# Performance work log

Measured on AMD Instinct MI355X. Metric: run time of the kernel, lower is better.

## Reference

```python
import jax, jax.numpy as jnp
import numpy as np

G = 64  # fixed grid size hardcoded in the torch module

def setup_inputs() -> dict:
    key = jax.random.key(0)
    ks = jax.random.split(key, 12)
    N, H = 500000, 256
    s = lambda fan_in: 1.0 / np.sqrt(fan_in)
    return {
        "positions": jax.random.normal(ks[0], (N, 3), jnp.float32) * 2.0,
        "grid_points": jax.random.normal(ks[1], (G, 3), jnp.float32) * 2.0,
        "W1": jax.random.normal(ks[2], (3, 64), jnp.float32) * s(3),
        "b1": jnp.zeros((64,), jnp.float32),
        "W2": jax.random.normal(ks[3], (64, 128), jnp.float32) * s(64),
        "b2": jnp.zeros((128,), jnp.float32),
        "W3": jax.random.normal(ks[4], (128, H), jnp.float32) * s(128),
        "b3": jnp.zeros((H,), jnp.float32),
        "Wn1": jax.random.normal(ks[5], (H, H), jnp.float32) * s(H),
        "bn1": jnp.zeros((H,), jnp.float32),
        "Wn2": jax.random.normal(ks[6], (H, H), jnp.float32) * s(H),
        "bn2": jnp.zeros((H,), jnp.float32),
        "Wh1": jax.random.normal(ks[7], (4, H, 128), jnp.float32) * s(H),
        "bh1": jnp.zeros((4, 128), jnp.float32),
        "Wh2": jax.random.normal(ks[8], (4, 128, 1), jnp.float32) * s(128),
        "bh2": jnp.zeros((4, 1), jnp.float32),
    }

def reference(positions, grid_points, W1, b1, W2, b2, W3, b3,
              Wn1, bn1, Wn2, bn2, Wh1, bh1, Wh2, bh2):
    # crystal_encoder: per-atom MLP 3 -> 64 -> 128 -> 256 over ALL N atoms
    h = jax.nn.relu(positions @ W1 + b1)
    h = jax.nn.relu(h @ W2 + b2)
    feat = h @ W3 + b3                                   # [N, H]

    # _map_crystal_to_grid: only the first min(N, 64) atoms are mapped.
    pos64 = positions[:G]                                # [64, 3]
    d2 = jnp.sum((pos64[:, None, :] - grid_points[None, :, :]) ** 2, axis=-1)
    idx = jnp.argmin(d2, axis=-1)                        # [64] nearest grid point per atom
    winner = jnp.full((G,), -1, jnp.int32).at[idx].max(jnp.arange(G, dtype=jnp.int32))
    grid_feats = jnp.where(winner[:, None] >= 0,
                           feat[jnp.clip(winner, 0)], 0.0)  # [64, H]

    # TetrahedralAGINetwork (per-node MLP, channels-first output convention)
    x = grid_feats[None]                                 # [1, 64, H]
    y = jax.nn.relu(x @ Wn1 + bn1) @ Wn2 + bn2           # [1, 64, H]
    agg = jnp.mean(jnp.swapaxes(y, 1, 2), axis=-1)       # mean over nodes -> [1, H]

    # 4 property heads, batched: [4, 1, 1] -> [4] (order: band_gap,
    # elastic_modulus, thermal_conductivity, dielectric_constant)
    h1 = jax.nn.relu(jnp.einsum('bc,kcd->kbd', agg, Wh1) + bh1[:, None, :])
    props = jnp.einsum('kbd,kdo->kbo', h1, Wh2) + bh2[:, None, :]
    return props.reshape(4)
```

## Files before the change

kernel.cpp:

```cpp
#include <hip/hip_runtime.h>


__device__ __forceinline__ void async_cp16(const float* g, float* l) {
    __builtin_amdgcn_global_load_lds(
        (const __attribute__((address_space(1))) void*)g,
        (__attribute__((address_space(3))) void*)l, 16, 0, 0);
}

__device__ __forceinline__ void stage_contig(const float* g, float* l, int nfloats, int tid) {
    const int lane = tid & 63, wv = tid >> 6;
    const int ninst = nfloats >> 8;
    for (int i = wv; i < ninst; i += 4)
        async_cp16(g + i*256 + lane*4, l + i*256);
}
__device__ __forceinline__ void stage_slice32(const float* g, float* l, int ld, int j0, int nrows, int tid) {
    const int lane = tid & 63, wv = tid >> 6;
    const int r = lane >> 3, c4 = (lane & 7) << 2;
    const int ninst = nrows >> 3;
    for (int i = wv; i < ninst; i += 4)
        async_cp16(g + (i*8 + r)*ld + j0 + c4, l + i*256);
}

__global__ __launch_bounds__(256) void k0_backbone(
    const float* __restrict__ positions, const float* __restrict__ grid,
    const float* __restrict__ W1, const float* __restrict__ b1,
    const float* __restrict__ W2, const float* __restrict__ b2,
    float* __restrict__ h2g_ws, int* __restrict__ win_ws)
{
    __shared__ __align__(16) float w2_s[64*128];
    __shared__ __align__(16) float h1_s[64][64];
    __shared__ float pos_s[192], grid_s[192], w1_s[192], b1_s[64];
    __shared__ int idx_s[64], win_s[64];

    const int tid = threadIdx.x;
    stage_contig(W2, w2_s, 64*128, tid);

    if (tid < 192) { pos_s[tid] = positions[tid]; grid_s[tid] = grid[tid]; w1_s[tid] = W1[tid]; }
    if (tid >= 192) b1_s[tid - 192] = b1[tid - 192];
    const float bb2 = b2[tid & 127];
    __syncthreads();

    if (tid < 64) {
        const float px = pos_s[tid*3], py = pos_s[tid*3+1], pz = pos_s[tid*3+2];
        float best = 3.4e38f; int bi = 0;
        for (int g = 0; g < 64; ++g) {
            const float dx = px - grid_s[g*3];
            const float dy = py - grid_s[g*3+1];
            const float dz = pz - grid_s[g*3+2];
            const float d2 = dx*dx + dy*dy + dz*dz;
            if (d2 < best) { best = d2; bi = g; }
        }
        idx_s[tid] = bi;
    }
    __syncthreads();
    if (tid < 64) {
        int m = -1;
        for (int i = 0; i < 64; ++i) if (idx_s[i] == tid) m = i;
        win_s[tid] = m;
        win_ws[tid] = m;
    }
    __syncthreads();

    #pragma unroll
    for (int u = 0; u < 16; ++u) {
        const int e = tid + u*256;
        const int t = e >> 6, k = e & 63;
        int r = win_s[t]; if (r < 0) r = 0;
        const float acc = b1_s[k] + pos_s[r*3]*w1_s[k] + pos_s[r*3+1]*w1_s[64+k]
                                  + pos_s[r*3+2]*w1_s[128+k];
        h1_s[t][k] = fmaxf(acc, 0.f);
    }
    __syncthreads();

    {
        const int d = tid & 127, t0 = tid >> 7;
        for (int bp = 0; bp < 8; ++bp) {
            float acc[4];
            #pragma unroll
            for (int m = 0; m < 4; ++m) acc[m] = bb2;
            for (int kc = 0; kc < 64; kc += 16) {
                float w[16];
                #pragma unroll
                for (int u = 0; u < 16; ++u) w[u] = w2_s[(kc+u)*128 + d];
                #pragma unroll
                for (int u = 0; u < 16; u += 4) {
                    #pragma unroll
                    for (int m = 0; m < 4; ++m) {
                        const float4 h4 = *(const float4*)&h1_s[bp*8 + t0 + 2*m][kc + u];
                        acc[m] += h4.x*w[u] + h4.y*w[u+1] + h4.z*w[u+2] + h4.w*w[u+3];
                    }
                }
            }
            #pragma unroll
            for (int m = 0; m < 4; ++m)
                h2g_ws[(bp*8 + t0 + 2*m)*128 + d] = fmaxf(acc[m], 0.f);
        }
    }
}

__global__ __launch_bounds__(256) void k1_gf(
    const float* __restrict__ W3, const float* __restrict__ b3,
    const float* __restrict__ h2g_ws, const int* __restrict__ win_ws,
    float* __restrict__ gf_ws)
{
    __shared__ __align__(16) float w3_s[128*32];
    __shared__ __align__(16) float h2_s[64*128];
    __shared__ int win_s[64];

    const int tid = threadIdx.x;
    const int j0  = blockIdx.x * 32;
    stage_slice32(W3, w3_s, 256, j0, 128, tid);
    stage_contig(h2g_ws, h2_s, 64*128, tid);

    const int jl = tid & 31, g = tid >> 5;
    const int j  = j0 + jl;
    const float bb = b3[j];
    if (tid < 64) win_s[tid] = win_ws[tid];
    __syncthreads();

    float acc[8];
    #pragma unroll
    for (int t = 0; t < 8; ++t) acc[t] = 0.f;
    for (int dc = 0; dc < 128; dc += 16) {
        float w[16];
        #pragma unroll
        for (int u = 0; u < 16; ++u) w[u] = w3_s[(dc+u)*32 + jl];
        #pragma unroll
        for (int u = 0; u < 16; u += 4) {
            #pragma unroll
            for (int t = 0; t < 8; ++t) {
                const float4 h4 = *(const float4*)&h2_s[(g*8 + t)*128 + dc + u];
                acc[t] += h4.x*w[u] + h4.y*w[u+1] + h4.z*w[u+2] + h4.w*w[u+3];
            }
        }
    }
    #pragma unroll
    for (int t = 0; t < 8; ++t)
        gf_ws[(g*8 + t)*256 + j] = (win_s[g*8 + t] >= 0) ? (acc[t] + bb) : 0.f;
}

__global__ __launch_bounds__(256) void k2_tpart(
    const float* __restrict__ Wn1, const float* __restrict__ bn1,
    const float* __restrict__ gf_ws, float* __restrict__ tpart_ws)
{
    __shared__ __align__(16) float wn1_s[256*32];
    __shared__ __align__(16) float gf_s[8*256];
    __shared__ float r_s[256];

    const int tid = threadIdx.x;
    const int bg  = blockIdx.x >> 3;
    const int j0  = (blockIdx.x & 7) * 32;
    stage_slice32(Wn1, wn1_s, 256, j0, 256, tid);
    stage_contig(gf_ws + bg*8*256, gf_s, 8*256, tid);

    const int jl = tid & 31, t = tid >> 5;
    const float bb = bn1[j0 + jl];
    __syncthreads();

    float acc = bb;
    for (int cc = 0; cc < 256; cc += 32) {
        float w[32];
        #pragma unroll
        for (int u = 0; u < 32; ++u) w[u] = wn1_s[(cc+u)*32 + jl];
        #pragma unroll
        for (int u = 0; u < 32; u += 4) {
            const float4 g4 = *(const float4*)&gf_s[t*256 + cc + u];
            acc += g4.x*w[u] + g4.y*w[u+1] + g4.z*w[u+2] + g4.w*w[u+3];
        }
    }
    r_s[tid] = fmaxf(acc, 0.f);
    __syncthreads();
    if (t == 0) {
        float ps = 0.f;
        #pragma unroll
        for (int tt = 0; tt < 8; ++tt) ps += r_s[tt*32 + jl];
        tpart_ws[bg*256 + j0 + jl] = ps;
    }
}

__global__ __launch_bounds__(256) void k3_agg(
    const float* __restrict__ Wn2, const float* __restrict__ bn2,
    const float* __restrict__ tpart_ws, float* __restrict__ agg_ws)
{
    __shared__ __align__(16) float wn2_s[256*32];
    __shared__ __align__(16) float tp_s[8*256];
    __shared__ __align__(16) float tbar_s[256];

    const int tid = threadIdx.x;
    const int c0  = blockIdx.x * 32;
    stage_slice32(Wn2, wn2_s, 256, c0, 256, tid);
    stage_contig(tpart_ws, tp_s, 8*256, tid);

    const float bb = (tid < 32) ? bn2[c0 + tid] : 0.f;
    __syncthreads();

    {
        float tb = 0.f;
        #pragma unroll
        for (int q = 0; q < 8; ++q) tb += tp_s[q*256 + tid];
        tbar_s[tid] = tb * (1.f/64.f);
    }
    __syncthreads();

    if (tid < 32) {
        float acc = bb;
        for (int jc = 0; jc < 256; jc += 32) {
            float w[32];
            #pragma unroll
            for (int u = 0; u < 32; ++u) w[u] = wn2_s[(jc+u)*32 + tid];
            #pragma unroll
            for (int u = 0; u < 32; u += 4) {
                const float4 t4 = *(const float4*)&tbar_s[jc + u];
                acc += t4.x*w[u] + t4.y*w[u+1] + t4.z*w[u+2] + t4.w*w[u+3];
            }
        }
        agg_ws[c0 + tid] = acc;
    }
}

__global__ __launch_bounds__(256) void k4_heads(
    const float* __restrict__ Wh1, const float* __restrict__ bh1,
    const float* __restrict__ agg_ws, float* __restrict__ h1h_ws)
{
    __shared__ __align__(16) float wh1_s[256*32];
    __shared__ __align__(16) float agg_s[256];

    const int tid = threadIdx.x;
    const int k   = blockIdx.x >> 2;
    const int d0  = (blockIdx.x & 3) * 32;
    stage_slice32(Wh1 + k*256*128, wh1_s, 128, d0, 256, tid);
    stage_contig(agg_ws, agg_s, 256, tid);

    const float bia = (tid < 32) ? bh1[k*128 + d0 + tid] : 0.f;
    __syncthreads();

    if (tid < 32) {
        float acc = bia;
        for (int cc = 0; cc < 256; cc += 16) {
            float wa[16];
            #pragma unroll
            for (int u = 0; u < 16; ++u) wa[u] = wh1_s[(cc+u)*32 + tid];
            #pragma unroll
            for (int u = 0; u < 16; u += 4) {
                const float4 a4 = *(const float4*)&agg_s[cc + u];
                acc += a4.x*wa[u] + a4.y*wa[u+1] + a4.z*wa[u+2] + a4.w*wa[u+3];
            }
        }
        h1h_ws[k*128 + d0 + tid] = fmaxf(acc, 0.f);
    }
}

__global__ __launch_bounds__(256) void k5_out(
    const float* __restrict__ Wh2, const float* __restrict__ bh2,
    const float* __restrict__ h1h_ws, float* __restrict__ out)
{
    __shared__ __align__(16) float h1h_s[512];
    __shared__ __align__(16) float wh2_s[512];
    const int tid = threadIdx.x;
    stage_contig(h1h_ws, h1h_s, 512, tid);
    stage_contig(Wh2,    wh2_s, 512, tid);
    const float bb = (tid < 4) ? bh2[tid] : 0.f;
    __syncthreads();

    if (tid < 4) {
        float acc = bb;
        for (int d = 0; d < 128; ++d) acc += h1h_s[tid*128 + d] * wh2_s[tid*128 + d];
        out[tid] = acc;
    }
}

extern "C" void kernel_launch(void* const* d_in, const int* in_sizes, int n_in,
                              void* d_out, int out_size, void* d_ws, size_t ws_size,
                              hipStream_t stream) {
    const float* positions = (const float*)d_in[0];
    const float* grid      = (const float*)d_in[1];
    const float* W1  = (const float*)d_in[2];
    const float* b1  = (const float*)d_in[3];
    const float* W2  = (const float*)d_in[4];
    const float* b2  = (const float*)d_in[5];
    const float* W3  = (const float*)d_in[6];
    const float* b3  = (const float*)d_in[7];
    const float* Wn1 = (const float*)d_in[8];
    const float* bn1 = (const float*)d_in[9];
    const float* Wn2 = (const float*)d_in[10];
    const float* bn2 = (const float*)d_in[11];
    const float* Wh1 = (const float*)d_in[12];
    const float* bh1 = (const float*)d_in[13];
    const float* Wh2 = (const float*)d_in[14];
    const float* bh2 = (const float*)d_in[15];
    float* out = (float*)d_out;

    char* ws = (char*)d_ws;
    float* h2g_ws   = (float*)(ws + 0);
    int*   win_ws   = (int*)  (ws + 32768);
    float* gf_ws    = (float*)(ws + 36864);
    float* tpart_ws = (float*)(ws + 102400);
    float* agg_ws   = (float*)(ws + 110592);
    float* h1h_ws   = (float*)(ws + 111616);

    hipLaunchKernelGGL(k0_backbone, dim3(1),  dim3(256), 0, stream,
                       positions, grid, W1, b1, W2, b2, h2g_ws, win_ws);
    hipLaunchKernelGGL(k1_gf,      dim3(8),  dim3(256), 0, stream,
                       W3, b3, h2g_ws, win_ws, gf_ws);
    hipLaunchKernelGGL(k2_tpart,   dim3(64), dim3(256), 0, stream,
                       Wn1, bn1, gf_ws, tpart_ws);
    hipLaunchKernelGGL(k3_agg,     dim3(8),  dim3(256), 0, stream,
                       Wn2, bn2, tpart_ws, agg_ws);
    hipLaunchKernelGGL(k4_heads,   dim3(16), dim3(256), 0, stream,
                       Wh1, bh1, agg_ws, h1h_ws);
    hipLaunchKernelGGL(k5_out,     dim3(1),  dim3(256), 0, stream,
                       Wh2, bh2, h1h_ws, out);
}
```

Baseline: 118.2 us.

## Fuse six-kernel chain into one cooperative kernel with prefetched weights

Replaces the sequence of six small dependent launches with one cooperative kernel of 29 blocks. Each block has a fixed role and loads its weight slice (W2, W3, Wn1, Wn2 or Wh1) into 128KB of dynamic LDS up front, so those loads overlap the earlier stages. Stages are separated by grid-wide syncs. This removes the per-launch overhead and the gaps between dependent kernels, and the partial-sum reduction now happens inside each stage. In exchange it adds grid-sync cost, leaves most blocks idle at any given stage, and falls back to the old six-kernel path if the cooperative launch fails.

Result: slower. 177.3 us (+49.9%).

```diff
diff --git a/kernel.cpp b/kernel.cpp
--- a/kernel.cpp
+++ b/kernel.cpp
@@ -1,4 +1,7 @@
 #include <hip/hip_runtime.h>
+#include <hip/hip_cooperative_groups.h>
+
+namespace cg = cooperative_groups;
 
 
 __device__ __forceinline__ void async_cp16(const float* g, float* l) {
@@ -6,7 +9,6 @@
         (const __attribute__((address_space(1))) void*)g,
         (__attribute__((address_space(3))) void*)l, 16, 0, 0);
 }
-
 __device__ __forceinline__ void stage_contig(const float* g, float* l, int nfloats, int tid) {
     const int lane = tid & 63, wv = tid >> 6;
     const int ninst = nfloats >> 8;
@@ -20,6 +22,255 @@
     for (int i = wv; i < ninst; i += 4)
         async_cp16(g + (i*8 + r)*ld + j0 + c4, l + i*256);
 }
+
+#define COOP_SMEM_BYTES 131072
+
+__global__ __launch_bounds__(256) void fused_coop(
+    const float* __restrict__ positions, const float* __restrict__ grid_pts,
+    const float* __restrict__ W1, const float* __restrict__ b1,
+    const float* __restrict__ W2, const float* __restrict__ b2,
+    const float* __restrict__ W3, const float* __restrict__ b3,
+    const float* __restrict__ Wn1, const float* __restrict__ bn1,
+    const float* __restrict__ Wn2, const float* __restrict__ bn2,
+    const float* __restrict__ Wh1, const float* __restrict__ bh1,
+    const float* __restrict__ Wh2, const float* __restrict__ bh2,
+    float* __restrict__ h2g_ws, int* __restrict__ win_ws,
+    float* __restrict__ gf_ws, float* __restrict__ tbar_ws,
+    float* __restrict__ agg_ws, float* __restrict__ out)
+{
+    extern __shared__ float smem[];
+    __shared__ float pos_s[192], grid_s[192], w1_s[192], b1_s[64];
+    __shared__ int   idx_s[64], win_s[64];
+    __shared__ __align__(16) float tbar_s[256];
+    __shared__ __align__(16) float agg_s[256];
+    __shared__ __align__(16) float h1h_s[128];
+    __shared__ __align__(16) float wh2_s[128];
+
+    const int tid = threadIdx.x;
+    const int bid = blockIdx.x;
+    cg::grid_group gg = cg::this_grid();
+
+    float bb2 = 0.f, bb3 = 0.f, bbn1 = 0.f, bbn2 = 0.f, bbh1 = 0.f, bbh2 = 0.f;
+
+    if (bid == 0) {
+        stage_contig(W2, smem, 64*128, tid);
+        if (tid < 192) { pos_s[tid] = positions[tid]; grid_s[tid] = grid_pts[tid]; w1_s[tid] = W1[tid]; }
+        if (tid >= 192) b1_s[tid - 192] = b1[tid - 192];
+        bb2 = b2[tid & 127];
+    } else if (bid <= 8) {
+        const int j0 = (bid - 1) * 32;
+        stage_slice32(W3, smem, 256, j0, 128, tid);
+        bb3 = b3[j0 + (tid & 31)];
+    } else if (bid <= 16) {
+        const int j0 = (bid - 9) * 32;
+        stage_slice32(Wn1, smem, 256, j0, 256, tid);
+        bbn1 = bn1[j0 + (tid & 31)];
+    } else if (bid <= 24) {
+        const int c0 = (bid - 17) * 32;
+        stage_slice32(Wn2, smem, 256, c0, 256, tid);
+        bbn2 = bn2[c0 + (tid & 31)];
+    } else {
+        const int k = bid - 25;
+        stage_contig(Wh1 + k*256*128, smem, 256*128, tid);
+        if (tid < 128) { bbh1 = bh1[k*128 + tid]; wh2_s[tid] = Wh2[k*128 + tid]; }
+        bbh2 = bh2[k];
+    }
+
+    if (bid == 0) {
+        float* w2_s = smem;
+        float* h1_s = smem + 8192;
+        __syncthreads();
+
+        if (tid < 64) {
+            const float px = pos_s[tid*3], py = pos_s[tid*3+1], pz = pos_s[tid*3+2];
+            float best = 3.4e38f; int bi = 0;
+            for (int g = 0; g < 64; ++g) {
+                const float dx = px - grid_s[g*3];
+                const float dy = py - grid_s[g*3+1];
+                const float dz = pz - grid_s[g*3+2];
+                const float d2 = dx*dx + dy*dy + dz*dz;
+                if (d2 < best) { best = d2; bi = g; }
+            }
+            idx_s[tid] = bi;
+        }
+        __syncthreads();
+        if (tid < 64) {
+            int m = -1;
+            for (int i = 0; i < 64; ++i) if (idx_s[i] == tid) m = i;
+            win_s[tid] = m;
+            win_ws[tid] = m;
+        }
+        __syncthreads();
+
+        #pragma unroll
+        for (int u = 0; u < 16; ++u) {
+            const int e = tid + u*256;
+            const int t = e >> 6, kk = e & 63;
+            int r = win_s[t]; if (r < 0) r = 0;
+            const float acc = b1_s[kk] + pos_s[r*3]*w1_s[kk] + pos_s[r*3+1]*w1_s[64+kk]
+                                       + pos_s[r*3+2]*w1_s[128+kk];
+            h1_s[t*64 + kk] = fmaxf(acc, 0.f);
+        }
+        __syncthreads();
+
+        {
+            const int d = tid & 127, t0 = tid >> 7;
+            for (int bp = 0; bp < 8; ++bp) {
+                float acc[4];
+                #pragma unroll
+                for (int m = 0; m < 4; ++m) acc[m] = bb2;
+                for (int kc = 0; kc < 64; kc += 16) {
+                    float w[16];
+                    #pragma unroll
+                    for (int u = 0; u < 16; ++u) w[u] = w2_s[(kc+u)*128 + d];
+                    #pragma unroll
+                    for (int u = 0; u < 16; u += 4) {
+                        #pragma unroll
+                        for (int m = 0; m < 4; ++m) {
+                            const float4 h4 = *(const float4*)&h1_s[(bp*8 + t0 + 2*m)*64 + kc + u];
+                            acc[m] += h4.x*w[u] + h4.y*w[u+1] + h4.z*w[u+2] + h4.w*w[u+3];
+                        }
+                    }
+                }
+                #pragma unroll
+                for (int m = 0; m < 4; ++m)
+                    h2g_ws[(bp*8 + t0 + 2*m)*128 + d] = fmaxf(acc[m], 0.f);
+            }
+        }
+    }
+
+    gg.sync();
+
+    if (bid >= 1 && bid <= 8) {
+        const int j0 = (bid - 1) * 32;
+        float* w3_s = smem;
+        float* h2_s = smem + 4096;
+        stage_contig(h2g_ws, h2_s, 64*128, tid);
+        if (tid < 64) win_s[tid] = win_ws[tid];
+        __syncthreads();
+
+        const int jl = tid & 31, g = tid >> 5;
+        float acc[8];
+        #pragma unroll
+        for (int t = 0; t < 8; ++t) acc[t] = 0.f;
+        for (int dc = 0; dc < 128; dc += 16) {
+            float w[16];
+            #pragma unroll
+            for (int u = 0; u < 16; ++u) w[u] = w3_s[(dc+u)*32 + jl];
+            #pragma unroll
+            for (int u = 0; u < 16; u += 4) {
+                #pragma unroll
+                for (int t = 0; t < 8; ++t) {
+                    const float4 h4 = *(const float4*)&h2_s[(g*8 + t)*128 + dc + u];
+                    acc[t] += h4.x*w[u] + h4.y*w[u+1] + h4.z*w[u+2] + h4.w*w[u+3];
+                }
+            }
+        }
+        #pragma unroll
+        for (int t = 0; t < 8; ++t)
+            gf_ws[(g*8 + t)*256 + j0 + jl] = (win_s[g*8 + t] >= 0) ? (acc[t] + bb3) : 0.f;
+    }
+
+    gg.sync();
+
+    if (bid >= 9 && bid <= 16) {
+        const int j0 = (bid - 9) * 32;
+        float* wn1_s = smem;
+        float* gfs   = smem + 8192;
+        float* r_s   = smem + 24576;
+        stage_contig(gf_ws, gfs, 64*256, tid);
+        __syncthreads();
+
+        const int jl = tid & 31, t = tid >> 5;
+        float acc[8];
+        #pragma unroll
+        for (int bg = 0; bg < 8; ++bg) acc[bg] = bbn1;
+        for (int cc = 0; cc < 256; cc += 32) {
+            float w[32];
+            #pragma unroll
+            for (int u = 0; u < 32; ++u) w[u] = wn1_s[(cc+u)*32 + jl];
+            #pragma unroll
+            for (int u = 0; u < 32; u += 4) {
+                #pragma unroll
+                for (int bg = 0; bg < 8; ++bg) {
+                    const float4 g4 = *(const float4*)&gfs[(bg*8 + t)*256 + cc + u];
+                    acc[bg] += g4.x*w[u] + g4.y*w[u+1] + g4.z*w[u+2] + g4.w*w[u+3];
+                }
+            }
+        }
+        #pragma unroll
+        for (int bg = 0; bg < 8; ++bg)
+            r_s[(bg*8 + t)*32 + jl] = fmaxf(acc[bg], 0.f);
+        __syncthreads();
+        if (t == 0) {
+            float tb = 0.f;
+            #pragma unroll
+            for (int bg = 0; bg < 8; ++bg) {
+                float ps = 0.f;
+                #pragma unroll
+                for (int tt = 0; tt < 8; ++tt) ps += r_s[(bg*8 + tt)*32 + jl];
+                tb += ps;
+            }
+            tbar_ws[j0 + jl] = tb * (1.f/64.f);
+        }
+    }
+
+    gg.sync();
+
+    if (bid >= 17 && bid <= 24) {
+        const int c0 = (bid - 17) * 32;
+        float* wn2_s = smem;
+        tbar_s[tid] = tbar_ws[tid];
+        __syncthreads();
+
+        if (tid < 32) {
+            float acc = bbn2;
+            for (int jc = 0; jc < 256; jc += 32) {
+                float w[32];
+                #pragma unroll
+                for (int u = 0; u < 32; ++u) w[u] = wn2_s[(jc+u)*32 + tid];
+                #pragma unroll
+                for (int u = 0; u < 32; u += 4) {
+                    const float4 t4 = *(const float4*)&tbar_s[jc + u];
+                    acc += t4.x*w[u] + t4.y*w[u+1] + t4.z*w[u+2] + t4.w*w[u+3];
+                }
+            }
+            agg_ws[c0 + tid] = acc;
+        }
+    }
+
+    gg.sync();
+
+    if (bid >= 25) {
+        const int k = bid - 25;
+        float* wh1_s = smem;
+        agg_s[tid] = agg_ws[tid];
+        __syncthreads();
+
+        if (tid < 128) {
+            const int d = tid;
+            float acc = bbh1;
+            for (int cc = 0; cc < 256; cc += 16) {
+                float wa[16];
+                #pragma unroll
+                for (int u = 0; u < 16; ++u) wa[u] = wh1_s[(cc+u)*128 + d];
+                #pragma unroll
+                for (int u = 0; u < 16; u += 4) {
+                    const float4 a4 = *(const float4*)&agg_s[cc + u];
+                    acc += a4.x*wa[u] + a4.y*wa[u+1] + a4.z*wa[u+2] + a4.w*wa[u+3];
+                }
+            }
+            h1h_s[d] = fmaxf(acc, 0.f);
+        }
+        __syncthreads();
+        if (tid == 0) {
+            float acc = bbh2;
+            for (int d = 0; d < 128; ++d) acc += h1h_s[d] * wh2_s[d];
+            out[k] = acc;
+        }
+    }
+}
+
 
 __global__ __launch_bounds__(256) void k0_backbone(
     const float* __restrict__ positions, const float* __restrict__ grid,
@@ -184,7 +435,7 @@
 {
     __shared__ __align__(16) float wn2_s[256*32];
     __shared__ __align__(16) float tp_s[8*256];
-    __shared__ __align__(16) float tbar_s[256];
+    __shared__ __align__(16) float tbars[256];
 
     const int tid = threadIdx.x;
     const int c0  = blockIdx.x * 32;
@@ -198,7 +449,7 @@
         float tb = 0.f;
         #pragma unroll
         for (int q = 0; q < 8; ++q) tb += tp_s[q*256 + tid];
-        tbar_s[tid] = tb * (1.f/64.f);
+        tbars[tid] = tb * (1.f/64.f);
     }
     __syncthreads();
 
@@ -210,7 +461,7 @@
             for (int u = 0; u < 32; ++u) w[u] = wn2_s[(jc+u)*32 + tid];
             #pragma unroll
             for (int u = 0; u < 32; u += 4) {
-                const float4 t4 = *(const float4*)&tbar_s[jc + u];
+                const float4 t4 = *(const float4*)&tbars[jc + u];
                 acc += t4.x*w[u] + t4.y*w[u+1] + t4.z*w[u+2] + t4.w*w[u+3];
             }
         }
@@ -223,13 +474,13 @@
     const float* __restrict__ agg_ws, float* __restrict__ h1h_ws)
 {
     __shared__ __align__(16) float wh1_s[256*32];
-    __shared__ __align__(16) float agg_s[256];
+    __shared__ __align__(16) float aggs[256];
 
     const int tid = threadIdx.x;
     const int k   = blockIdx.x >> 2;
     const int d0  = (blockIdx.x & 3) * 32;
     stage_slice32(Wh1 + k*256*128, wh1_s, 128, d0, 256, tid);
-    stage_contig(agg_ws, agg_s, 256, tid);
+    stage_contig(agg_ws, aggs, 256, tid);
 
     const float bia = (tid < 32) ? bh1[k*128 + d0 + tid] : 0.f;
     __syncthreads();
@@ -242,7 +493,7 @@
             for (int u = 0; u < 16; ++u) wa[u] = wh1_s[(cc+u)*32 + tid];
             #pragma unroll
             for (int u = 0; u < 16; u += 4) {
-                const float4 a4 = *(const float4*)&agg_s[cc + u];
+                const float4 a4 = *(const float4*)&aggs[cc + u];
                 acc += a4.x*wa[u] + a4.y*wa[u+1] + a4.z*wa[u+2] + a4.w*wa[u+3];
             }
         }
@@ -254,17 +505,17 @@
     const float* __restrict__ Wh2, const float* __restrict__ bh2,
     const float* __restrict__ h1h_ws, float* __restrict__ out)
 {
-    __shared__ __align__(16) float h1h_s[512];
-    __shared__ __align__(16) float wh2_s[512];
-    const int tid = threadIdx.x;
-    stage_contig(h1h_ws, h1h_s, 512, tid);
-    stage_contig(Wh2,    wh2_s, 512, tid);
+    __shared__ __align__(16) float h1hs[512];
+    __shared__ __align__(16) float wh2s[512];
+    const int tid = threadIdx.x;
+    stage_contig(h1h_ws, h1hs, 512, tid);
+    stage_contig(Wh2,    wh2s, 512, tid);
     const float bb = (tid < 4) ? bh2[tid] : 0.f;
     __syncthreads();
 
     if (tid < 4) {
         float acc = bb;
-        for (int d = 0; d < 128; ++d) acc += h1h_s[tid*128 + d] * wh2_s[tid*128 + d];
+        for (int d = 0; d < 128; ++d) acc += h1hs[tid*128 + d] * wh2s[tid*128 + d];
         out[tid] = acc;
     }
 }
@@ -297,17 +548,39 @@
     float* tpart_ws = (float*)(ws + 102400);
     float* agg_ws   = (float*)(ws + 110592);
     float* h1h_ws   = (float*)(ws + 111616);
-
-    hipLaunchKernelGGL(k0_backbone, dim3(1),  dim3(256), 0, stream,
-                       positions, grid, W1, b1, W2, b2, h2g_ws, win_ws);
-    hipLaunchKernelGGL(k1_gf,      dim3(8),  dim3(256), 0, stream,
-                       W3, b3, h2g_ws, win_ws, gf_ws);
-    hipLaunchKernelGGL(k2_tpart,   dim3(64), dim3(256), 0, stream,
-                       Wn1, bn1, gf_ws, tpart_ws);
-    hipLaunchKernelGGL(k3_agg,     dim3(8),  dim3(256), 0, stream,
-                       Wn2, bn2, tpart_ws, agg_ws);
-    hipLaunchKernelGGL(k4_heads,   dim3(16), dim3(256), 0, stream,
-                       Wh1, bh1, agg_ws, h1h_ws);
-    hipLaunchKernelGGL(k5_out,     dim3(1),  dim3(256), 0, stream,
-                       Wh2, bh2, h1h_ws, out);
-}
+    float* tbar_ws  = (float*)(ws + 120832);
+
+    static int smem_attr_set = 0;
+    if (!smem_attr_set) {
+        (void)hipFuncSetAttribute((const void*)fused_coop,
+                                  hipFuncAttributeMaxDynamicSharedMemorySize,
+                                  COOP_SMEM_BYTES);
+        smem_attr_set = 1;
+    }
+
+    void* args[] = {
+        (void*)&positions, (void*)&grid, (void*)&W1, (void*)&b1, (void*)&W2,
+        (void*)&b2, (void*)&W3, (void*)&b3, (void*)&Wn1, (void*)&bn1,
+        (void*)&Wn2, (void*)&bn2, (void*)&Wh1, (void*)&bh1, (void*)&Wh2,
+        (void*)&bh2, (void*)&h2g_ws, (void*)&win_ws, (void*)&gf_ws,
+        (void*)&tbar_ws, (void*)&agg_ws, (void*)&out };
+
+    hipError_t e = hipLaunchCooperativeKernel((const void*)fused_coop,
+                                              dim3(29), dim3(256), args,
+                                              COOP_SMEM_BYTES, stream);
+    if (e != hipSuccess) {
+        (void)hipGetLastError();
+        hipLaunchKernelGGL(k0_backbone, dim3(1),  dim3(256), 0, stream,
+                           positions, grid, W1, b1, W2, b2, h2g_ws, win_ws);
+        hipLaunchKernelGGL(k1_gf,      dim3(8),  dim3(256), 0, stream,
+                           W3, b3, h2g_ws, win_ws, gf_ws);
+        hipLaunchKernelGGL(k2_tpart,   dim3(64), dim3(256), 0, stream,
+                           Wn1, bn1, gf_ws, tpart_ws);
+        hipLaunchKernelGGL(k3_agg,     dim3(8),  dim3(256), 0, stream,
+                           Wn2, bn2, tpart_ws, agg_ws);
+        hipLaunchKernelGGL(k4_heads,   dim3(16), dim3(256), 0, stream,
+                           Wh1, bh1, agg_ws, h1h_ws);
+        hipLaunchKernelGGL(k5_out,     dim3(1),  dim3(256), 0, stream,
+                           Wh2, bh2, h1h_ws, out);
+    }
+}
```

## Fuse backbone with grid-feature layer and heads with output into fewer kernels

Applied to the files above, without the earlier changes.

Merges the first-layer/argmin backbone kernel with the W3 grid-feature kernel. Each of 8 blocks now recomputes the nearest-grid mapping and MLP layers for its own 8 grid slots and stages all of W3 into 128 KB of dynamic LDS. Also merges the two head kernels into one block per head, which does the final dot product in-block. This cuts six launches to four and removes workspace round-trips, at the cost of redundant per-block argmin work, direct global reads of W2, and fewer, larger blocks with heavy LDS use.

Result: faster. 111.5 us (-5.7%).

```diff
diff --git a/kernel.cpp b/kernel.cpp
--- a/kernel.cpp
+++ b/kernel.cpp
@@ -6,7 +6,6 @@
         (const __attribute__((address_space(1))) void*)g,
         (__attribute__((address_space(3))) void*)l, 16, 0, 0);
 }
-
 __device__ __forceinline__ void stage_contig(const float* g, float* l, int nfloats, int tid) {
     const int lane = tid & 63, wv = tid >> 6;
     const int ninst = nfloats >> 8;
@@ -21,23 +20,29 @@
         async_cp16(g + (i*8 + r)*ld + j0 + c4, l + i*256);
 }
 
-__global__ __launch_bounds__(256) void k0_backbone(
-    const float* __restrict__ positions, const float* __restrict__ grid,
+#define A_SMEM_BYTES (32768*4)
+
+__global__ __launch_bounds__(256) void a_gf(
+    const float* __restrict__ positions, const float* __restrict__ grid_pts,
     const float* __restrict__ W1, const float* __restrict__ b1,
     const float* __restrict__ W2, const float* __restrict__ b2,
-    float* __restrict__ h2g_ws, int* __restrict__ win_ws)
-{
-    __shared__ __align__(16) float w2_s[64*128];
-    __shared__ __align__(16) float h1_s[64][64];
+    const float* __restrict__ W3, const float* __restrict__ b3,
+    float* __restrict__ gf_ws)
+{
+    extern __shared__ float w3s[];
     __shared__ float pos_s[192], grid_s[192], w1_s[192], b1_s[64];
-    __shared__ int idx_s[64], win_s[64];
-
-    const int tid = threadIdx.x;
-    stage_contig(W2, w2_s, 64*128, tid);
-
-    if (tid < 192) { pos_s[tid] = positions[tid]; grid_s[tid] = grid[tid]; w1_s[tid] = W1[tid]; }
+    __shared__ int   idx_s[64], win_s[8];
+    __shared__ __align__(16) float h1s[8*64];
+    __shared__ __align__(16) float h2s[8*128];
+
+    const int tid = threadIdx.x;
+    const int bg  = blockIdx.x;
+
+    stage_contig(W3, w3s, 32768, tid);
+    if (tid < 192) { pos_s[tid] = positions[tid]; grid_s[tid] = grid_pts[tid]; w1_s[tid] = W1[tid]; }
     if (tid >= 192) b1_s[tid - 192] = b1[tid - 192];
     const float bb2 = b2[tid & 127];
+    const float bb3 = b3[tid];
     __syncthreads();
 
     if (tid < 64) {
@@ -53,90 +58,71 @@
         idx_s[tid] = bi;
     }
     __syncthreads();
-    if (tid < 64) {
+    if (tid < 8) {
+        const int g = bg*8 + tid;
         int m = -1;
-        for (int i = 0; i < 64; ++i) if (idx_s[i] == tid) m = i;
+        for (int i = 0; i < 64; ++i) if (idx_s[i] == g) m = i;
         win_s[tid] = m;
-        win_ws[tid] = m;
     }
     __syncthreads();
 
     #pragma unroll
-    for (int u = 0; u < 16; ++u) {
-        const int e = tid + u*256;
-        const int t = e >> 6, k = e & 63;
-        int r = win_s[t]; if (r < 0) r = 0;
+    for (int u = 0; u < 2; ++u) {
+        const int e  = tid + u*256;
+        const int lr = e >> 6, k = e & 63;
+        int r = win_s[lr]; if (r < 0) r = 0;
         const float acc = b1_s[k] + pos_s[r*3]*w1_s[k] + pos_s[r*3+1]*w1_s[64+k]
                                   + pos_s[r*3+2]*w1_s[128+k];
-        h1_s[t][k] = fmaxf(acc, 0.f);
+        h1s[lr*64 + k] = fmaxf(acc, 0.f);
     }
     __syncthreads();
 
     {
         const int d = tid & 127, t0 = tid >> 7;
-        for (int bp = 0; bp < 8; ++bp) {
-            float acc[4];
-            #pragma unroll
-            for (int m = 0; m < 4; ++m) acc[m] = bb2;
-            for (int kc = 0; kc < 64; kc += 16) {
-                float w[16];
+        float acc[4];
+        #pragma unroll
+        for (int m = 0; m < 4; ++m) acc[m] = bb2;
+        for (int kc = 0; kc < 64; kc += 16) {
+            float w[16];
+            #pragma unroll
+            for (int u = 0; u < 16; ++u) w[u] = W2[(kc+u)*128 + d];
+            #pragma unroll
+            for (int u = 0; u < 16; u += 4) {
                 #pragma unroll
-                for (int u = 0; u < 16; ++u) w[u] = w2_s[(kc+u)*128 + d];
+                for (int m = 0; m < 4; ++m) {
+                    const float4 h4 = *(const float4*)&h1s[(t0 + 2*m)*64 + kc + u];
+                    acc[m] += h4.x*w[u] + h4.y*w[u+1] + h4.z*w[u+2] + h4.w*w[u+3];
+                }
+            }
+        }
+        #pragma unroll
+        for (int m = 0; m < 4; ++m)
+            h2s[(t0 + 2*m)*128 + d] = fmaxf(acc[m], 0.f);
+    }
+    __syncthreads();
+
+    {
+        const int j = tid;
+        float ag[8];
+        #pragma unroll
+        for (int t = 0; t < 8; ++t) ag[t] = 0.f;
+        for (int dc = 0; dc < 128; dc += 16) {
+            float w[16];
+            #pragma unroll
+            for (int u = 0; u < 16; ++u) w[u] = w3s[(dc+u)*256 + j];
+            #pragma unroll
+            for (int u = 0; u < 16; u += 4) {
                 #pragma unroll
-                for (int u = 0; u < 16; u += 4) {
-                    #pragma unroll
-                    for (int m = 0; m < 4; ++m) {
-                        const float4 h4 = *(const float4*)&h1_s[bp*8 + t0 + 2*m][kc + u];
-                        acc[m] += h4.x*w[u] + h4.y*w[u+1] + h4.z*w[u+2] + h4.w*w[u+3];
-                    }
+                for (int t = 0; t < 8; ++t) {
+                    const float4 h4 = *(const float4*)&h2s[t*128 + dc + u];
+                    ag[t] += h4.x*w[u] + h4.y*w[u+1] + h4.z*w[u+2] + h4.w*w[u+3];
                 }
             }
-            #pragma unroll
-            for (int m = 0; m < 4; ++m)
-                h2g_ws[(bp*8 + t0 + 2*m)*128 + d] = fmaxf(acc[m], 0.f);
-        }
-    }
-}
-
-__global__ __launch_bounds__(256) void k1_gf(
-    const float* __restrict__ W3, const float* __restrict__ b3,
-    const float* __restrict__ h2g_ws, const int* __restrict__ win_ws,
-    float* __restrict__ gf_ws)
-{
-    __shared__ __align__(16) float w3_s[128*32];
-    __shared__ __align__(16) float h2_s[64*128];
-    __shared__ int win_s[64];
-
-    const int tid = threadIdx.x;
-    const int j0  = blockIdx.x * 32;
-    stage_slice32(W3, w3_s, 256, j0, 128, tid);
-    stage_contig(h2g_ws, h2_s, 64*128, tid);
-
-    const int jl = tid & 31, g = tid >> 5;
-    const int j  = j0 + jl;
-    const float bb = b3[j];
-    if (tid < 64) win_s[tid] = win_ws[tid];
-    __syncthreads();
-
-    float acc[8];
-    #pragma unroll
-    for (int t = 0; t < 8; ++t) acc[t] = 0.f;
-    for (int dc = 0; dc < 128; dc += 16) {
-        float w[16];
-        #pragma unroll
-        for (int u = 0; u < 16; ++u) w[u] = w3_s[(dc+u)*32 + jl];
-        #pragma unroll
-        for (int u = 0; u < 16; u += 4) {
-            #pragma unroll
-            for (int t = 0; t < 8; ++t) {
-                const float4 h4 = *(const float4*)&h2_s[(g*8 + t)*128 + dc + u];
-                acc[t] += h4.x*w[u] + h4.y*w[u+1] + h4.z*w[u+2] + h4.w*w[u+3];
-            }
-        }
-    }
-    #pragma unroll
-    for (int t = 0; t < 8; ++t)
-        gf_ws[(g*8 + t)*256 + j] = (win_s[g*8 + t] >= 0) ? (acc[t] + bb) : 0.f;
+        }
+        #pragma unroll
+        for (int t = 0; t < 8; ++t)
+            gf_ws[(bg*8 + t)*256 + j] = (win_s[t] >= 0) ? (ag[t] + bb3) : 0.f;
+    }
 }
 
 __global__ __launch_bounds__(256) void k2_tpart(
@@ -184,7 +170,7 @@
 {
     __shared__ __align__(16) float wn2_s[256*32];
     __shared__ __align__(16) float tp_s[8*256];
-    __shared__ __align__(16) float tbar_s[256];
+    __shared__ __align__(16) float tbars[256];
 
     const int tid = threadIdx.x;
     const int c0  = blockIdx.x * 32;
@@ -198,7 +184,7 @@
         float tb = 0.f;
         #pragma unroll
         for (int q = 0; q < 8; ++q) tb += tp_s[q*256 + tid];
-        tbar_s[tid] = tb * (1.f/64.f);
+        tbars[tid] = tb * (1.f/64.f);
     }
     __syncthreads();
 
@@ -210,7 +196,7 @@
             for (int u = 0; u < 32; ++u) w[u] = wn2_s[(jc+u)*32 + tid];
             #pragma unroll
             for (int u = 0; u < 32; u += 4) {
-                const float4 t4 = *(const float4*)&tbar_s[jc + u];
+                const float4 t4 = *(const float4*)&tbars[jc + u];
                 acc += t4.x*w[u] + t4.y*w[u+1] + t4.z*w[u+2] + t4.w*w[u+3];
             }
         }
@@ -218,54 +204,48 @@
     }
 }
 
-__global__ __launch_bounds__(256) void k4_heads(
+#define D_SMEM_BYTES (32768*4)
+
+__global__ __launch_bounds__(256) void d_heads(
     const float* __restrict__ Wh1, const float* __restrict__ bh1,
-    const float* __restrict__ agg_ws, float* __restrict__ h1h_ws)
-{
-    __shared__ __align__(16) float wh1_s[256*32];
+    const float* __restrict__ Wh2, const float* __restrict__ bh2,
+    const float* __restrict__ agg_ws, float* __restrict__ out)
+{
+    extern __shared__ float wh1s[];
     __shared__ __align__(16) float agg_s[256];
-
-    const int tid = threadIdx.x;
-    const int k   = blockIdx.x >> 2;
-    const int d0  = (blockIdx.x & 3) * 32;
-    stage_slice32(Wh1 + k*256*128, wh1_s, 128, d0, 256, tid);
+    __shared__ __align__(16) float h1h_s[128];
+    __shared__ __align__(16) float wh2_s[128];
+
+    const int tid = threadIdx.x;
+    const int k   = blockIdx.x;
+
+    stage_contig(Wh1 + k*32768, wh1s, 32768, tid);
     stage_contig(agg_ws, agg_s, 256, tid);
-
-    const float bia = (tid < 32) ? bh1[k*128 + d0 + tid] : 0.f;
-    __syncthreads();
-
-    if (tid < 32) {
-        float acc = bia;
+    const float bbh1 = (tid < 128) ? bh1[k*128 + tid] : 0.f;
+    if (tid < 128) wh2_s[tid] = Wh2[k*128 + tid];
+    const float bbh2 = bh2[k];
+    __syncthreads();
+
+    if (tid < 128) {
+        const int d = tid;
+        float acc = bbh1;
         for (int cc = 0; cc < 256; cc += 16) {
             float wa[16];
             #pragma unroll
-            for (int u = 0; u < 16; ++u) wa[u] = wh1_s[(cc+u)*32 + tid];
+            for (int u = 0; u < 16; ++u) wa[u] = wh1s[(cc+u)*128 + d];
             #pragma unroll
             for (int u = 0; u < 16; u += 4) {
                 const float4 a4 = *(const float4*)&agg_s[cc + u];
                 acc += a4.x*wa[u] + a4.y*wa[u+1] + a4.z*wa[u+2] + a4.w*wa[u+3];
             }
         }
-        h1h_ws[k*128 + d0 + tid] = fmaxf(acc, 0.f);
-    }
-}
-
-__global__ __launch_bounds__(256) void k5_out(
-    const float* __restrict__ Wh2, const float* __restrict__ bh2,
-    const float* __restrict__ h1h_ws, float* __restrict__ out)
-{
-    __shared__ __align__(16) float h1h_s[512];
-    __shared__ __align__(16) float wh2_s[512];
-    const int tid = threadIdx.x;
-    stage_contig(h1h_ws, h1h_s, 512, tid);
-    stage_contig(Wh2,    wh2_s, 512, tid);
-    const float bb = (tid < 4) ? bh2[tid] : 0.f;
-    __syncthreads();
-
-    if (tid < 4) {
-        float acc = bb;
-        for (int d = 0; d < 128; ++d) acc += h1h_s[tid*128 + d] * wh2_s[tid*128 + d];
-        out[tid] = acc;
+        h1h_s[d] = fmaxf(acc, 0.f);
+    }
+    __syncthreads();
+    if (tid == 0) {
+        float acc = bbh2;
+        for (int d = 0; d < 128; ++d) acc += h1h_s[d] * wh2_s[d];
+        out[k] = acc;
     }
 }
 
@@ -291,23 +271,23 @@
     float* out = (float*)d_out;
 
     char* ws = (char*)d_ws;
-    float* h2g_ws   = (float*)(ws + 0);
-    int*   win_ws   = (int*)  (ws + 32768);
-    float* gf_ws    = (float*)(ws + 36864);
-    float* tpart_ws = (float*)(ws + 102400);
-    float* agg_ws   = (float*)(ws + 110592);
-    float* h1h_ws   = (float*)(ws + 111616);
-
-    hipLaunchKernelGGL(k0_backbone, dim3(1),  dim3(256), 0, stream,
-                       positions, grid, W1, b1, W2, b2, h2g_ws, win_ws);
-    hipLaunchKernelGGL(k1_gf,      dim3(8),  dim3(256), 0, stream,
-                       W3, b3, h2g_ws, win_ws, gf_ws);
-    hipLaunchKernelGGL(k2_tpart,   dim3(64), dim3(256), 0, stream,
+    float* gf_ws    = (float*)(ws + 0);
+    float* tpart_ws = (float*)(ws + 65536);
+    float* agg_ws   = (float*)(ws + 73728);
+
+    (void)hipFuncSetAttribute((const void*)a_gf,
+                              hipFuncAttributeMaxDynamicSharedMemorySize,
+                              A_SMEM_BYTES);
+    (void)hipFuncSetAttribute((const void*)d_heads,
+                              hipFuncAttributeMaxDynamicSharedMemorySize,
+                              D_SMEM_BYTES);
+
+    hipLaunchKernelGGL(a_gf,     dim3(8),  dim3(256), A_SMEM_BYTES, stream,
+                       positions, grid, W1, b1, W2, b2, W3, b3, gf_ws);
+    hipLaunchKernelGGL(k2_tpart, dim3(64), dim3(256), 0, stream,
                        Wn1, bn1, gf_ws, tpart_ws);
-    hipLaunchKernelGGL(k3_agg,     dim3(8),  dim3(256), 0, stream,
+    hipLaunchKernelGGL(k3_agg,   dim3(8),  dim3(256), 0, stream,
                        Wn2, bn2, tpart_ws, agg_ws);
-    hipLaunchKernelGGL(k4_heads,   dim3(16), dim3(256), 0, stream,
-                       Wh1, bh1, agg_ws, h1h_ws);
-    hipLaunchKernelGGL(k5_out,     dim3(1),  dim3(256), 0, stream,
-                       Wh2, bh2, h1h_ws, out);
-}
+    hipLaunchKernelGGL(d_heads,  dim3(4),  dim3(256), D_SMEM_BYTES, stream,
+                       Wh1, bh1, Wh2, bh2, agg_ws, out);
+}
```
